# Kernel optimization log

Hardware: AMD Instinct MI355X
Metric: run time of the kernel (lower is better)

Reference implementation:

```python
import jax, jax.numpy as jnp
import numpy as np

N_NODES = 50000
N_EDGES = 800000
IN_CH = 128
OUT_CH = 64
HEADS = 8


def setup_inputs() -> dict:
    key = jax.random.key(0)
    k1, k2, k3, k4 = jax.random.split(key, 4)
    x = jax.random.normal(k1, (N_NODES, IN_CH), dtype=jnp.float32)
    edge_index = jax.random.randint(k2, (2, N_EDGES), 0, N_NODES, dtype=jnp.int32)
    # xavier-uniform-ish scale
    W = jax.random.normal(k3, (IN_CH, OUT_CH), dtype=jnp.float32) * (1.0 / np.sqrt(IN_CH))
    attn_weights = jax.random.normal(k4, (2 * OUT_CH, 1), dtype=jnp.float32) * (1.0 / np.sqrt(2 * OUT_CH))
    return {"x": x, "edge_index": edge_index, "W": W, "attn_weights": attn_weights}


def reference(x, edge_index, W, attn_weights):
    # h: [N, out]
    h = x @ W
    ei, ej = edge_index[0], edge_index[1]
    h_i = h[ei]                      # [E, out] gather by destination
    h_j = h[ej]                      # [E, out] gather by source
    edge_feat = jnp.concatenate([h_i, h_j], axis=-1)  # [E, 2*out]
    logits = jax.nn.leaky_relu(edge_feat @ attn_weights, negative_slope=0.2)  # [E, 1]
    # NOTE: original does softmax over dim=0 -> GLOBAL softmax over all edges
    alpha = jax.nn.softmax(logits, axis=0)  # [E, 1]
    # dropout p=0.6 is a no-op in eval mode (training=False)
    msg = h_j * alpha                # [E, out]
    h_head = jnp.zeros_like(h).at[ei].add(msg)  # scatter-add into destinations
    # All heads share W and attn_weights (see source loop), so with dropout off
    # every head is identical; concat == tile along feature dim.
    return jnp.tile(h_head, (1, HEADS))  # [N, out*heads]
```

## Files before the change

kernel.cpp:

```cpp
#include <hip/hip_runtime.h>

#define N_NODES 50000
#define N_EDGES 800000
#define IN_CH 128
#define OUT_CH 64
#define HEADS 8
#define ROW 512
#define NBLK_G 782
#define NBLK_A 782
#define NBIN 196
#define BINCAP 4608
#define MAXDEG 64
#define WS_STRIDE 136

typedef float f4 __attribute__((ext_vector_type(4)));
typedef short bf16x8 __attribute__((ext_vector_type(8)));

__device__ __forceinline__ float lrelu(float z) {
    return z > 0.0f ? z : 0.2f * z;
}

__device__ __forceinline__ unsigned f2b(float f) {
    unsigned u = __float_as_uint(f);
    return (u + 0x7FFFu + ((u >> 16) & 1u)) >> 16;
}

__global__ __launch_bounds__(256) void gemm_bin(const float* __restrict__ x,
                                                const float* __restrict__ W,
                                                const float* __restrict__ attn,
                                                const int4* __restrict__ ei4,
                                                const int4* __restrict__ ej4,
                                                unsigned short* __restrict__ hbuf,
                                                float* __restrict__ s,
                                                float* __restrict__ t,
                                                int* __restrict__ bin_count,
                                                unsigned* __restrict__ binned) {
    __shared__ unsigned short xs[64 * WS_STRIDE];
    __shared__ unsigned short wls[64 * WS_STRIDE];
    const int tid = threadIdx.x;
    const int bid = blockIdx.x;

    if (bid & 1) {
        unsigned* hist = (unsigned*)xs;
        unsigned* bse  = hist + NBIN;
        unsigned* cur  = bse + NBIN;
        if (tid < NBIN) { hist[tid] = 0u; cur[tid] = 0u; }
        __syncthreads();
        const int g = (bid >> 1) * 256 + tid;
        const bool act = g < N_EDGES / 4;
        int4 li = make_int4(0, 0, 0, 0), lj = make_int4(0, 0, 0, 0);
        if (act) {
            li = ei4[g];
            lj = ej4[g];
            atomicAdd(&hist[li.x >> 8], 1u);
            atomicAdd(&hist[li.y >> 8], 1u);
            atomicAdd(&hist[li.z >> 8], 1u);
            atomicAdd(&hist[li.w >> 8], 1u);
        }
        __syncthreads();
        if (tid < NBIN) {
            const unsigned c = hist[tid];
            bse[tid] = c ? (unsigned)atomicAdd(&bin_count[tid], (int)c) : 0u;
        }
        __syncthreads();
        if (act) {
            const unsigned p0 = bse[li.x >> 8] + atomicAdd(&cur[li.x >> 8], 1u);
            if (p0 < BINCAP) binned[(li.x >> 8) * BINCAP + p0] =
                ((unsigned)(li.x & 255) << 16) | (unsigned)lj.x;
            const unsigned p1 = bse[li.y >> 8] + atomicAdd(&cur[li.y >> 8], 1u);
            if (p1 < BINCAP) binned[(li.y >> 8) * BINCAP + p1] =
                ((unsigned)(li.y & 255) << 16) | (unsigned)lj.y;
            const unsigned p2 = bse[li.z >> 8] + atomicAdd(&cur[li.z >> 8], 1u);
            if (p2 < BINCAP) binned[(li.z >> 8) * BINCAP + p2] =
                ((unsigned)(li.z & 255) << 16) | (unsigned)lj.z;
            const unsigned p3 = bse[li.w >> 8] + atomicAdd(&cur[li.w >> 8], 1u);
            if (p3 < BINCAP) binned[(li.w >> 8) * BINCAP + p3] =
                ((unsigned)(li.w & 255) << 16) | (unsigned)lj.w;
        }
        return;
    }

    const int base = (bid >> 1) * 64;
    {
        const float4* W4 = (const float4*)W;
#pragma unroll
        for (int j = 0; j < 8; ++j) {
            const int idx = tid + j * 256;
            const int k = idx >> 4;
            const int c = (idx & 15) * 4;
            const float4 v = W4[idx];
            wls[(c + 0) * WS_STRIDE + k] = (unsigned short)f2b(v.x);
            wls[(c + 1) * WS_STRIDE + k] = (unsigned short)f2b(v.y);
            wls[(c + 2) * WS_STRIDE + k] = (unsigned short)f2b(v.z);
            wls[(c + 3) * WS_STRIDE + k] = (unsigned short)f2b(v.w);
        }
    }
    {
        const float4* x4 = (const float4*)x;
#pragma unroll
        for (int j = 0; j < 8; ++j) {
            const int idx = tid + j * 256;
            const int r = idx >> 5;
            const int kq = idx & 31;
            const int row = base + r;
            float4 v = make_float4(0.f, 0.f, 0.f, 0.f);
            if (row < N_NODES) v = x4[row * 32 + kq];
            ushort4 pb;
            pb.x = (unsigned short)f2b(v.x);
            pb.y = (unsigned short)f2b(v.y);
            pb.z = (unsigned short)f2b(v.z);
            pb.w = (unsigned short)f2b(v.w);
            *(ushort4*)&xs[r * WS_STRIDE + kq * 4] = pb;
        }
    }
    __syncthreads();
    const int w = tid >> 6, lane = tid & 63;
    const int m = lane & 15;
    const int kq = lane >> 4;
    bf16x8 afr[4];
#pragma unroll
    for (int kb = 0; kb < 4; ++kb)
        afr[kb] = *(const bf16x8*)&xs[(w * 16 + m) * WS_STRIDE + kb * 32 + kq * 8];
    float sacc[4] = {0.f, 0.f, 0.f, 0.f};
    float tacc[4] = {0.f, 0.f, 0.f, 0.f};
#pragma unroll
    for (int ct = 0; ct < 4; ++ct) {
        f4 acc = {0.f, 0.f, 0.f, 0.f};
#pragma unroll
        for (int kb = 0; kb < 4; ++kb) {
            const bf16x8 b = *(const bf16x8*)&wls[(ct * 16 + m) * WS_STRIDE + kb * 32 + kq * 8];
            acc = __builtin_amdgcn_mfma_f32_16x16x32_bf16(afr[kb], b, acc, 0, 0, 0);
        }
        const float a1 = attn[ct * 16 + m];
        const float a2 = attn[64 + ct * 16 + m];
#pragma unroll
        for (int r = 0; r < 4; ++r) {
            sacc[r] = fmaf(acc[r], a1, sacc[r]);
            tacc[r] = fmaf(acc[r], a2, tacc[r]);
            const int row = base + w * 16 + kq * 4 + r;
            if (row < N_NODES)
                hbuf[row * OUT_CH + ct * 16 + m] = (unsigned short)f2b(acc[r]);
        }
    }
#pragma unroll
    for (int off = 1; off < 16; off <<= 1) {
#pragma unroll
        for (int r = 0; r < 4; ++r) {
            sacc[r] += __shfl_xor(sacc[r], off, 64);
            tacc[r] += __shfl_xor(tacc[r], off, 64);
        }
    }
    if (m == 0) {
#pragma unroll
        for (int r = 0; r < 4; ++r) {
            const int row = base + w * 16 + kq * 4 + r;
            if (row < N_NODES) { s[row] = sacc[r]; t[row] = tacc[r]; }
        }
    }
}

__global__ __launch_bounds__(1024) void weight_pass(const unsigned* __restrict__ binned,
                                                    const int* __restrict__ bin_count,
                                                    const float* __restrict__ s,
                                                    const float* __restrict__ t,
                                                    unsigned* __restrict__ cv,
                                                    int* __restrict__ count,
                                                    float* __restrict__ Zsum) {
    __shared__ unsigned bkt[256 * MAXDEG];
    __shared__ unsigned cnt_l[256];
    __shared__ float s_l[256];
    __shared__ float red[16];
    const int tid = threadIdx.x;
    const int bin = blockIdx.x;
    if (tid < 256) {
        cnt_l[tid] = 0u;
        const int d = bin * 256 + tid;
        s_l[tid] = (d < N_NODES) ? s[d] : 0.0f;
    }
    __syncthreads();
    int n = bin_count[bin];
    if (n > BINCAP) n = BINCAP;
    float zs = 0.0f;
    for (int i = tid; i < n; i += 1024) {
        const unsigned e = binned[bin * BINCAP + i];
        const int dl = (int)((e >> 16) & 255u);
        const int src = (int)(e & 0xFFFFu);
        const float w = __expf(lrelu(s_l[dl] + t[src]));
        zs += w;
        const unsigned r = atomicAdd(&cnt_l[dl], 1u);
        if (r < MAXDEG) bkt[dl * MAXDEG + r] = (f2b(w) << 16) | (unsigned)src;
    }
    __syncthreads();
    {
        uint4* cv4 = (uint4*)(cv + bin * (256 * MAXDEG));
        const uint4* b4 = (const uint4*)bkt;
        for (int i = tid; i < 4096; i += 1024) cv4[i] = b4[i];
    }
    if (tid < 256) {
        const int d = bin * 256 + tid;
        if (d < N_NODES) count[d] = (int)cnt_l[tid];
    }
#pragma unroll
    for (int off = 32; off > 0; off >>= 1)
        zs += __shfl_down(zs, off, 64);
    if ((tid & 63) == 0) red[tid >> 6] = zs;
    __syncthreads();
    if (tid == 0) {
        float v = 0.0f;
#pragma unroll
        for (int k = 0; k < 16; ++k) v += red[k];
        atomicAdd(Zsum, v);
    }
}

__global__ __launch_bounds__(256) void gather_out(const int* __restrict__ count,
                                                  const unsigned* __restrict__ cv,
                                                  const float* __restrict__ Zsum,
                                                  const unsigned short* __restrict__ hbuf,
                                                  float* __restrict__ out) {
    const int n = blockIdx.x * 4 + (threadIdx.x >> 6);
    const int lane = threadIdx.x & 63;
    const int slot = lane >> 3;
    const int q = lane & 7;
    const float z = 1.0f / Zsum[0];
    int cnt = count[n];
    cnt = cnt < MAXDEG ? cnt : MAXDEG;
    const int base = n * MAXDEG;
    const uint4* h4 = (const uint4*)hbuf;
    f4 a0 = (f4)(0.0f);
    f4 a1 = (f4)(0.0f);
    unsigned pk = 0u;
    if (slot < cnt) pk = cv[base + slot];
    uint4 hv = h4[(int)(pk & 0xFFFFu) * 8 + q];
    for (int i = 0; i < cnt; i += 8) {
        unsigned pk_n = 0u;
        const int ee = i + 8 + slot;
        if (ee < cnt) pk_n = cv[base + ee];
        const uint4 hv_n = h4[(int)(pk_n & 0xFFFFu) * 8 + q];
        const float w = __uint_as_float(pk & 0xFFFF0000u);
        a0.x = fmaf(w, __uint_as_float(hv.x << 16),        a0.x);
        a0.y = fmaf(w, __uint_as_float(hv.x & 0xFFFF0000u), a0.y);
        a0.z = fmaf(w, __uint_as_float(hv.y << 16),        a0.z);
        a0.w = fmaf(w, __uint_as_float(hv.y & 0xFFFF0000u), a0.w);
        a1.x = fmaf(w, __uint_as_float(hv.z << 16),        a1.x);
        a1.y = fmaf(w, __uint_as_float(hv.z & 0xFFFF0000u), a1.y);
        a1.z = fmaf(w, __uint_as_float(hv.w << 16),        a1.z);
        a1.w = fmaf(w, __uint_as_float(hv.w & 0xFFFF0000u), a1.w);
        pk = pk_n;
        hv = hv_n;
    }
#pragma unroll
    for (int off = 8; off <= 32; off <<= 1) {
        a0.x += __shfl_xor(a0.x, off, 64);
        a0.y += __shfl_xor(a0.y, off, 64);
        a0.z += __shfl_xor(a0.z, off, 64);
        a0.w += __shfl_xor(a0.w, off, 64);
        a1.x += __shfl_xor(a1.x, off, 64);
        a1.y += __shfl_xor(a1.y, off, 64);
        a1.z += __shfl_xor(a1.z, off, 64);
        a1.w += __shfl_xor(a1.w, off, 64);
    }
    a0 *= z;
    a1 *= z;
    f4* out4 = (f4*)out;
    const int ob = n * 128 + slot * 16 + q * 2;
    __builtin_nontemporal_store(a0, out4 + ob);
    __builtin_nontemporal_store(a1, out4 + ob + 1);
}

extern "C" void kernel_launch(void* const* d_in, const int* in_sizes, int n_in,
                              void* d_out, int out_size, void* d_ws, size_t ws_size,
                              hipStream_t stream) {
    const float* x    = (const float*)d_in[0];
    const int*   eidx = (const int*)d_in[1];
    const float* W    = (const float*)d_in[2];
    const float* attn = (const float*)d_in[3];
    float* out = (float*)d_out;

    unsigned short* hbuf = (unsigned short*)d_ws;
    unsigned* cv     = (unsigned*)(hbuf + N_NODES * OUT_CH);
    unsigned* binned = cv + NBIN * 256 * MAXDEG;
    float* s         = (float*)(binned + NBIN * BINCAP);
    float* t         = s + N_NODES;
    int* count       = (int*)(t + N_NODES);
    int* bin_count   = count + N_NODES;
    float* Zsum      = (float*)(bin_count + NBIN);

    const int4* ei4 = (const int4*)eidx;
    const int4* ej4 = (const int4*)(eidx + N_EDGES);

    hipMemsetAsync(bin_count, 0, (NBIN + 1) * sizeof(int), stream);
    gemm_bin   <<<NBLK_G + NBLK_A, 256, 0, stream>>>(x, W, attn, ei4, ej4,
                                                     hbuf, s, t, bin_count, binned);
    weight_pass<<<NBIN, 1024, 0, stream>>>(binned, bin_count, s, t, cv, count, Zsum);
    gather_out <<<N_NODES / 4, 256, 0, stream>>>(count, cv, Zsum, hbuf, out);
}
```

Before: 171.3 us.

## Replace global bin atomics with per-cell local sort and offset table

The binning blocks now compute an in-block prefix scan of the bin histogram, sort their 1024 edges locally in shared memory, write them out contiguously per cell, and record per-cell bin offsets. This removes the global atomics on bin counts and the scattered writes into fixed-capacity bins, and the BINCAP truncation goes away. The weight pass then has each of 782 threads walk one cell's segment for its bin. That gives short serial loops with poor load balance and reads of scattered small segments.

```diff
diff --git a/kernel.cpp b/kernel.cpp
--- a/kernel.cpp
+++ b/kernel.cpp
@@ -8,8 +8,9 @@
 #define ROW 512
 #define NBLK_G 782
 #define NBLK_A 782
+#define NCELL 782
 #define NBIN 196
-#define BINCAP 4608
+#define BOFS_STRIDE 200
 #define MAXDEG 64
 #define WS_STRIDE 136
 
@@ -33,7 +34,7 @@
                                                 unsigned short* __restrict__ hbuf,
                                                 float* __restrict__ s,
                                                 float* __restrict__ t,
-                                                int* __restrict__ bin_count,
+                                                unsigned short* __restrict__ bofs,
                                                 unsigned* __restrict__ binned) {
     __shared__ unsigned short xs[64 * WS_STRIDE];
     __shared__ unsigned short wls[64 * WS_STRIDE];
@@ -42,11 +43,14 @@
 
     if (bid & 1) {
         unsigned* hist = (unsigned*)xs;
-        unsigned* bse  = hist + NBIN;
-        unsigned* cur  = bse + NBIN;
-        if (tid < NBIN) { hist[tid] = 0u; cur[tid] = 0u; }
-        __syncthreads();
-        const int g = (bid >> 1) * 256 + tid;
+        unsigned* cur  = hist + 256;
+        unsigned* wsum = cur + 256;
+        unsigned* lbuf = wsum + 8;
+        const int lane = tid & 63, wid = tid >> 6;
+        hist[tid] = 0u;
+        __syncthreads();
+        const int cell = bid >> 1;
+        const int g = cell * 256 + tid;
         const bool act = g < N_EDGES / 4;
         int4 li = make_int4(0, 0, 0, 0), lj = make_int4(0, 0, 0, 0);
         if (act) {
@@ -58,24 +62,36 @@
             atomicAdd(&hist[li.w >> 8], 1u);
         }
         __syncthreads();
-        if (tid < NBIN) {
-            const unsigned c = hist[tid];
-            bse[tid] = c ? (unsigned)atomicAdd(&bin_count[tid], (int)c) : 0u;
-        }
+        const unsigned h = (tid < NBIN) ? hist[tid] : 0u;
+        unsigned v = h;
+        for (int o = 1; o < 64; o <<= 1) {
+            const unsigned u = __shfl_up(v, o, 64);
+            if (lane >= o) v += u;
+        }
+        if (lane == 63) wsum[wid] = v;
+        __syncthreads();
+        unsigned basep = 0;
+        for (int k = 0; k < wid; ++k) basep += wsum[k];
+        const unsigned excl = basep + v - h;
+        if (tid <= NBIN) bofs[cell * BOFS_STRIDE + tid] = (unsigned short)excl;
+        cur[tid] = excl;
         __syncthreads();
         if (act) {
-            const unsigned p0 = bse[li.x >> 8] + atomicAdd(&cur[li.x >> 8], 1u);
-            if (p0 < BINCAP) binned[(li.x >> 8) * BINCAP + p0] =
-                ((unsigned)(li.x & 255) << 16) | (unsigned)lj.x;
-            const unsigned p1 = bse[li.y >> 8] + atomicAdd(&cur[li.y >> 8], 1u);
-            if (p1 < BINCAP) binned[(li.y >> 8) * BINCAP + p1] =
-                ((unsigned)(li.y & 255) << 16) | (unsigned)lj.y;
-            const unsigned p2 = bse[li.z >> 8] + atomicAdd(&cur[li.z >> 8], 1u);
-            if (p2 < BINCAP) binned[(li.z >> 8) * BINCAP + p2] =
-                ((unsigned)(li.z & 255) << 16) | (unsigned)lj.z;
-            const unsigned p3 = bse[li.w >> 8] + atomicAdd(&cur[li.w >> 8], 1u);
-            if (p3 < BINCAP) binned[(li.w >> 8) * BINCAP + p3] =
-                ((unsigned)(li.w & 255) << 16) | (unsigned)lj.w;
+            unsigned p;
+            p = atomicAdd(&cur[li.x >> 8], 1u);
+            lbuf[p] = ((unsigned)(li.x & 255) << 16) | (unsigned)lj.x;
+            p = atomicAdd(&cur[li.y >> 8], 1u);
+            lbuf[p] = ((unsigned)(li.y & 255) << 16) | (unsigned)lj.y;
+            p = atomicAdd(&cur[li.z >> 8], 1u);
+            lbuf[p] = ((unsigned)(li.z & 255) << 16) | (unsigned)lj.z;
+            p = atomicAdd(&cur[li.w >> 8], 1u);
+            lbuf[p] = ((unsigned)(li.w & 255) << 16) | (unsigned)lj.w;
+        }
+        __syncthreads();
+        {
+            uint4* d4 = (uint4*)&binned[(unsigned)cell * 1024];
+            const uint4* s4 = (const uint4*)lbuf;
+            d4[tid] = s4[tid];
         }
         return;
     }
@@ -160,7 +176,7 @@
 }
 
 __global__ __launch_bounds__(1024) void weight_pass(const unsigned* __restrict__ binned,
-                                                    const int* __restrict__ bin_count,
+                                                    const unsigned short* __restrict__ bofs,
                                                     const float* __restrict__ s,
                                                     const float* __restrict__ t,
                                                     unsigned* __restrict__ cv,
@@ -178,17 +194,20 @@
         s_l[tid] = (d < N_NODES) ? s[d] : 0.0f;
     }
     __syncthreads();
-    int n = bin_count[bin];
-    if (n > BINCAP) n = BINCAP;
     float zs = 0.0f;
-    for (int i = tid; i < n; i += 1024) {
-        const unsigned e = binned[bin * BINCAP + i];
-        const int dl = (int)((e >> 16) & 255u);
-        const int src = (int)(e & 0xFFFFu);
-        const float w = __expf(lrelu(s_l[dl] + t[src]));
-        zs += w;
-        const unsigned r = atomicAdd(&cnt_l[dl], 1u);
-        if (r < MAXDEG) bkt[dl * MAXDEG + r] = (f2b(w) << 16) | (unsigned)src;
+    if (tid < NCELL) {
+        const int st = (int)bofs[tid * BOFS_STRIDE + bin];
+        const int en = (int)bofs[tid * BOFS_STRIDE + bin + 1];
+        const unsigned* cp = &binned[(unsigned)tid * 1024];
+        for (int i = st; i < en; ++i) {
+            const unsigned e = cp[i];
+            const int dl = (int)((e >> 16) & 255u);
+            const int src = (int)(e & 0xFFFFu);
+            const float w = __expf(lrelu(s_l[dl] + t[src]));
+            zs += w;
+            const unsigned r = atomicAdd(&cnt_l[dl], 1u);
+            if (r < MAXDEG) bkt[dl * MAXDEG + r] = (f2b(w) << 16) | (unsigned)src;
+        }
     }
     __syncthreads();
     {
@@ -280,18 +299,18 @@
     unsigned short* hbuf = (unsigned short*)d_ws;
     unsigned* cv     = (unsigned*)(hbuf + N_NODES * OUT_CH);
     unsigned* binned = cv + NBIN * 256 * MAXDEG;
-    float* s         = (float*)(binned + NBIN * BINCAP);
+    unsigned short* bofs = (unsigned short*)(binned + NCELL * 1024);
+    float* s         = (float*)(bofs + NCELL * BOFS_STRIDE);
     float* t         = s + N_NODES;
     int* count       = (int*)(t + N_NODES);
-    int* bin_count   = count + N_NODES;
-    float* Zsum      = (float*)(bin_count + NBIN);
+    float* Zsum      = (float*)(count + N_NODES);
 
     const int4* ei4 = (const int4*)eidx;
     const int4* ej4 = (const int4*)(eidx + N_EDGES);
 
-    hipMemsetAsync(bin_count, 0, (NBIN + 1) * sizeof(int), stream);
+    hipMemsetAsync(Zsum, 0, sizeof(float), stream);
     gemm_bin   <<<NBLK_G + NBLK_A, 256, 0, stream>>>(x, W, attn, ei4, ej4,
-                                                     hbuf, s, t, bin_count, binned);
-    weight_pass<<<NBIN, 1024, 0, stream>>>(binned, bin_count, s, t, cv, count, Zsum);
+                                                     hbuf, s, t, bofs, binned);
+    weight_pass<<<NBIN, 1024, 0, stream>>>(binned, bofs, s, t, cv, count, Zsum);
     gather_out <<<N_NODES / 4, 256, 0, stream>>>(count, cv, Zsum, hbuf, out);
 }
```

Measured after the change: 176.7 us. 1.03x slower.
